# Kernel tuning notes

Hardware: AMD Instinct MI355X
Metric: run time of the kernel (lower is better)

The kernel has to match this reference:

```python
import jax, jax.numpy as jnp
import numpy as np

C = 512
GROUPS = 32
EPS = 1e-6


def setup_inputs() -> dict:
    key = jax.random.key(0)
    ks = jax.random.split(key, 10)
    s = 0.02
    return {
        "x": jax.random.normal(ks[0], (2, C, 64, 64), dtype=jnp.float32),
        "gn_scale": jnp.ones((C,), jnp.float32),
        "gn_bias": jnp.zeros((C,), jnp.float32),
        "wq": jax.random.normal(ks[1], (C, C), jnp.float32) * s,
        "bq": jnp.zeros((C,), jnp.float32),
        "wk": jax.random.normal(ks[2], (C, C), jnp.float32) * s,
        "bk": jnp.zeros((C,), jnp.float32),
        "wv": jax.random.normal(ks[3], (C, C), jnp.float32) * s,
        "bv": jnp.zeros((C,), jnp.float32),
        "wo": jax.random.normal(ks[4], (C, C), jnp.float32) * s,
        "bo": jnp.zeros((C,), jnp.float32),
    }


def group_norm(x, scale, bias):
    # x: [b, c, h, w]; 32 groups over channel dim
    b, c, h, w = x.shape
    xg = x.reshape(b, GROUPS, c // GROUPS, h, w)
    mean = jnp.mean(xg, axis=(2, 3, 4), keepdims=True)
    var = jnp.var(xg, axis=(2, 3, 4), keepdims=True)
    xg = (xg - mean) * jax.lax.rsqrt(var + EPS)
    x = xg.reshape(b, c, h, w)
    return x * scale[None, :, None, None] + bias[None, :, None, None]


def reference(x, gn_scale, gn_bias, wq, bq, wk, bk, wv, bv, wo, bo):
    b, c, h, w = x.shape
    n = h * w
    hn = group_norm(x, gn_scale, gn_bias).reshape(b, c, n)  # [b,c,n]
    # 1x1 conv == channel matmul: out[b,o,n] = W[o,i] @ h[b,i,n] + bias
    q = jnp.einsum('oi,bin->bon', wq, hn) + bq[None, :, None]
    k = jnp.einsum('oi,bin->bon', wk, hn) + bk[None, :, None]
    v = jnp.einsum('oi,bin->bon', wv, hn) + bv[None, :, None]
    # weight[b, i, j] = q_i . k_j, softmax over j
    scale = int(c) ** (-0.5)
    weight = jnp.einsum('bci,bcj->bij', q, k) * scale  # [b,n,n]
    weight = jax.nn.softmax(weight, axis=2)
    # h[b,c,i] = sum_j v[b,c,j] * weight[b,i,j]
    out = jnp.einsum('bcj,bij->bci', v, weight)
    out = jnp.einsum('oi,bin->bon', wo, out) + bo[None, :, None]
    return out.reshape(b, c, h, w) + x
```

## Files before the change

kernel.cpp:

```cpp
#include <hip/hip_runtime.h>
#include <hip/hip_bf16.h>


typedef __attribute__((ext_vector_type(8))) short short8_t;
typedef __attribute__((ext_vector_type(4))) short short4_t;
typedef __attribute__((ext_vector_type(4))) float f32x4;

__device__ __forceinline__ void gload16(const void* g, void* l) {
  __builtin_amdgcn_global_load_lds(
      (const __attribute__((address_space(1))) void*)g,
      (__attribute__((address_space(3))) void*)l, 16, 0, 0);
}

__device__ __forceinline__ short f2bf_bits(float f) {
  __hip_bfloat16 h = __float2bfloat16(f);
  return *reinterpret_cast<short*>(&h);
}
__device__ __forceinline__ float bfbits2f(short s) {
  union { unsigned int u; float f; } c;
  c.u = ((unsigned int)(unsigned short)s) << 16;
  return c.f;
}

__global__ __launch_bounds__(512)
void s_gemm8(const __hip_bfloat16* __restrict__ qk,
             __hip_bfloat16* __restrict__ P, float* __restrict__ part2,
             float c)
{
  const long long QKz = 4096LL * 1024;
  const long long SS  = 4096LL * 4096;

  const int b = blockIdx.x;
  const int bz = b >> 8;
  const int r = b & 255, xcd = r & 7, sl = r >> 3;
  const int bm = (xcd >> 1) * 4 + (sl & 3);
  const int bn = (xcd & 1) * 8 + (sl >> 2);

  const __hip_bfloat16* Aq = qk + (size_t)bz * QKz;
  const __hip_bfloat16* Bk = Aq + 512;

  const int tid = threadIdx.x;
  const int wid = tid >> 6, l = tid & 63;
  const int wrM = wid >> 2, wcN = wid & 3;
  const int lhi = l >> 4, llo = l & 15;

  __shared__ char sm[2 * 65536];

  f32x4 acc[2][2][4][2] = {};
  short8_t af[4][2], bf[2][2];

  const int rIn = l >> 3;
  const int colSw = 8 * ((l & 7) ^ (rIn & 7));
  const __hip_bfloat16* gA = Aq + (size_t)(bm * 256 + rIn) * 1024 + colSw;
  const __hip_bfloat16* gB = Bk + (size_t)(bn * 256 + rIn) * 1024 + colSw;

  auto STG = [&](int mat, int half, int t) {
    const __hip_bfloat16* src = mat ? gB : gA;
    char* dst = sm + (t & 1) * 65536 + mat * 32768;
    const int rb = half * 128 + wid * 16;
    gload16(src + (size_t)rb * 1024 + t * 64, dst + rb * 128);
    gload16(src + (size_t)(rb + 8) * 1024 + t * 64, dst + (rb + 8) * 128);
  };

#define PHASE(MH, NH, LA, LB, VM, ...) do {                                   \
    const char* bbA = sm + bsel * 65536;                                      \
    const char* bbB = bbA + 32768;                                            \
    if (LA) {                                                                 \
      _Pragma("unroll") for (int m = 0; m < 4; ++m) {                         \
        const int rowA = (MH) * 128 + wrM * 64 + m * 16 + llo;                \
        _Pragma("unroll") for (int kk = 0; kk < 2; ++kk)                      \
          af[m][kk] = *(const short8_t*)(bbA + rowA * 128 +                   \
                        (((kk * 4 + lhi) ^ (rowA & 7)) * 16));                \
      }                                                                       \
    }                                                                         \
    if (LB) {                                                                 \
      _Pragma("unroll") for (int n = 0; n < 2; ++n) {                         \
        const int rowB = (NH) * 128 + wcN * 32 + n * 16 + llo;                \
        _Pragma("unroll") for (int kk = 0; kk < 2; ++kk)                      \
          bf[n][kk] = *(const short8_t*)(bbB + rowB * 128 +                   \
                        (((kk * 4 + lhi) ^ (rowB & 7)) * 16));                \
      }                                                                       \
    }                                                                         \
    __VA_ARGS__;                                                              \
    __builtin_amdgcn_s_barrier();                                             \
    __builtin_amdgcn_s_setprio(1);                                            \
    _Pragma("unroll") for (int kk = 0; kk < 2; ++kk)                          \
      _Pragma("unroll") for (int m = 0; m < 4; ++m)                           \
        _Pragma("unroll") for (int n = 0; n < 2; ++n)                         \
          acc[MH][NH][m][n] = __builtin_amdgcn_mfma_f32_16x16x32_bf16(        \
              af[m][kk], bf[n][kk], acc[MH][NH][m][n], 0, 0, 0);              \
    __builtin_amdgcn_s_setprio(0);                                            \
    if ((VM) == 1) asm volatile("s_waitcnt vmcnt(4)" ::: "memory");           \
    if ((VM) == 2) asm volatile("s_waitcnt vmcnt(0)" ::: "memory");           \
    __builtin_amdgcn_s_barrier();                                             \
  } while (0)

  STG(0, 0, 0); STG(1, 0, 0); STG(0, 1, 0); STG(1, 1, 0);
  STG(0, 0, 1); STG(1, 0, 1); STG(0, 1, 1); STG(1, 1, 1);
  asm volatile("s_waitcnt vmcnt(0)" ::: "memory");
  __builtin_amdgcn_s_barrier();

  for (int t = 0; t < 8; ++t) {
    const int bsel = t & 1;
    const int stB = (t >= 1 && t < 7);
    const int stA = (t < 6);
    const int vm = (t < 6) ? 1 : (t == 6) ? 2 : 0;
    PHASE(0, 0, 1, 1, 0, if (stB) { STG(1, 0, t + 1); STG(1, 1, t + 1); });
    PHASE(0, 1, 0, 1, 0, if (stA) STG(0, 0, t + 2););
    PHASE(1, 1, 1, 0, 0, );
    PHASE(1, 0, 0, 1, vm, if (stA) STG(0, 1, t + 2););
  }
#undef PHASE

  __hip_bfloat16* Pb = P + (size_t)bz * SS;
  float rp[2][4][4];
#pragma unroll
  for (int Mh = 0; Mh < 2; ++Mh)
#pragma unroll
    for (int m = 0; m < 4; ++m)
#pragma unroll
      for (int rr = 0; rr < 4; ++rr) {
        const int grow = bm * 256 + Mh * 128 + wrM * 64 + m * 16 + lhi * 4 + rr;
        float s = 0.f;
#pragma unroll
        for (int Nh = 0; Nh < 2; ++Nh)
#pragma unroll
          for (int n = 0; n < 2; ++n) {
            const int gcol = bn * 256 + Nh * 128 + wcN * 32 + n * 16 + llo;
            const float v = exp2f(acc[Mh][Nh][m][n][rr] * c);
            Pb[(size_t)grow * 4096 + gcol] = __float2bfloat16(v);
            s += v;
          }
        rp[Mh][m][rr] = s;
      }
#pragma unroll
  for (int Mh = 0; Mh < 2; ++Mh)
#pragma unroll
    for (int m = 0; m < 4; ++m)
#pragma unroll
      for (int rr = 0; rr < 4; ++rr) {
        float s = rp[Mh][m][rr];
        s += __shfl_xor(s, 1); s += __shfl_xor(s, 2);
        s += __shfl_xor(s, 4); s += __shfl_xor(s, 8);
        rp[Mh][m][rr] = s;
      }
  __syncthreads();
  float* rsl = (float*)sm;
  if (llo == 0) {
#pragma unroll
    for (int Mh = 0; Mh < 2; ++Mh)
#pragma unroll
      for (int m = 0; m < 4; ++m)
#pragma unroll
        for (int rr = 0; rr < 4; ++rr) {
          const int rl = Mh * 128 + wrM * 64 + m * 16 + lhi * 4 + rr;
          rsl[rl * 4 + wcN] = rp[Mh][m][rr];
        }
  }
  __syncthreads();
  if (tid < 256) {
    const float s = rsl[tid * 4] + rsl[tid * 4 + 1] + rsl[tid * 4 + 2] + rsl[tid * 4 + 3];
    part2[((size_t)bz * 16 + bn) * 4096 + bm * 256 + tid] = s;
  }
}

__global__ __launch_bounds__(256)
void rs_final(const float* __restrict__ part2, float* __restrict__ rs)
{
  const int i = blockIdx.x * 256 + threadIdx.x;
  const int z = i >> 12, row = i & 4095;
  float s = 0.f;
#pragma unroll
  for (int bn = 0; bn < 16; ++bn)
    s += part2[((size_t)z * 16 + bn) * 4096 + row];
  rs[(size_t)z * 4096 + row] = 1.f / s;
}

template<int OUTF, int BIASMODE, int RESID, int PIPE, int MF, int NORM>
__device__ __forceinline__ void gemm_body(
    const __hip_bfloat16* __restrict__ A,
    const __hip_bfloat16* __restrict__ B,
    void* __restrict__ Cv,
    const float* __restrict__ bias,
    const float* __restrict__ resid,
    const float* __restrict__ rn,
    float scale, int K, int lda, int ldb, int ldc,
    long long strC, long long strR,
    int bm, int bn, int z, char* sm)
{
  constexpr int BUFSZ = MF * 4096 + 16384;
  const int tid = threadIdx.x;
  const int w = tid >> 6, l = tid & 63;
  const int wr = w >> 1, wc = w & 1;
  const int lhi = l >> 4, llo = l & 15;
  const int m0 = bm * (MF * 32), n0 = bn * 128;

  f32x4 acc[MF][4] = {};

  const int rowInCh = l >> 3;
  const int colOff = 8 * ((l & 7) ^ (rowInCh & 7));

  const __hip_bfloat16* gAr[MF];
  const __hip_bfloat16* gBr[4];
#pragma unroll
  for (int j = 0; j < MF; ++j)
    gAr[j] = A + (size_t)(m0 + w * (8 * MF) + j * 8 + rowInCh) * lda + colOff;
#pragma unroll
  for (int r = 0; r < 4; ++r)
    gBr[r] = B + (size_t)(n0 + w * 32 + r * 8 + rowInCh) * ldb + colOff;

  auto stage = [&](int kt, int buf) {
    char* sA = sm + buf * BUFSZ;
    char* sB = sA + MF * 4096;
    const int ko = kt * 64;
#pragma unroll
    for (int j = 0; j < MF; ++j)
      gload16(gAr[j] + ko, sA + (w * MF + j) * 1024);
#pragma unroll
    for (int r = 0; r < 4; ++r)
      gload16(gBr[r] + ko, sB + (w * 4 + r) * 1024);
  };

  auto compute = [&](int buf) {
    char* sA = sm + buf * BUFSZ;
    char* sB = sA + MF * 4096;
#pragma unroll
    for (int kk = 0; kk < 2; ++kk) {
      short8_t af[MF], bfv[4];
#pragma unroll
      for (int m = 0; m < MF; ++m) {
        const int row = wr * (16 * MF) + m * 16 + llo;
        const int inner = ((kk * 4 + lhi) ^ (row & 7)) * 16;
        af[m] = *(const short8_t*)(sA + row * 128 + inner);
      }
#pragma unroll
      for (int n = 0; n < 4; ++n) {
        const int row = wc * 64 + n * 16 + llo;
        const int inner = ((kk * 4 + lhi) ^ (row & 7)) * 16;
        bfv[n] = *(const short8_t*)(sB + row * 128 + inner);
      }
#pragma unroll
      for (int m = 0; m < MF; ++m)
#pragma unroll
        for (int n = 0; n < 4; ++n)
          acc[m][n] = __builtin_amdgcn_mfma_f32_16x16x32_bf16(af[m], bfv[n], acc[m][n], 0, 0, 0);
    }
  };

  const int nkt = K >> 6;
  if (PIPE) {
    stage(0, 0);
    __syncthreads();
    int cur = 0;
    for (int kt = 0; kt < nkt; ++kt) {
      if (kt + 1 < nkt) stage(kt + 1, cur ^ 1);
      compute(cur);
      __syncthreads();
      cur ^= 1;
    }
  } else {
    for (int kt = 0; kt < nkt; ++kt) {
      __syncthreads();
      stage(kt, 0);
      __syncthreads();
      compute(0);
    }
  }

#pragma unroll
  for (int m = 0; m < MF; ++m) {
#pragma unroll
    for (int r = 0; r < 4; ++r) {
      const int grow = m0 + wr * (16 * MF) + m * 16 + lhi * 4 + r;
#pragma unroll
      for (int n = 0; n < 4; ++n) {
        const int gcol = n0 + wc * 64 + n * 16 + llo;
        float v = acc[m][n][r] * scale;
        if (NORM == 1) v *= rn[(size_t)z * 4096 + gcol];
        if (BIASMODE == 1) v += bias[grow];
        if (BIASMODE == 2) v += bias[gcol];
        const size_t idx = (size_t)z * strC + (size_t)grow * ldc + gcol;
        if (RESID) v += resid[(size_t)z * strR + (size_t)grow * ldc + gcol];
        if (OUTF == 0) ((__hip_bfloat16*)Cv)[idx] = __float2bfloat16(v);
        else           ((float*)Cv)[idx] = v;
      }
    }
  }
}

template<int OUTF, int BIASMODE, int RESID, int PIPE, int SWZ, int MF, int NORM>
__global__ __launch_bounds__(256, 2)
void gemm_nt(const __hip_bfloat16* __restrict__ A,
             const __hip_bfloat16* __restrict__ B,
             void* __restrict__ Cv,
             const float* __restrict__ bias,
             const float* __restrict__ resid,
             const float* __restrict__ rn,
             float scale, int M, int N, int K,
             int lda, int ldb, int ldc,
             long long strA, long long strB, long long strC, long long strR)
{
  int bm, bn, bz;
  if (SWZ == 0) {
    bm = blockIdx.x; bn = blockIdx.y; bz = blockIdx.z;
  } else if (SWZ == 2) {
    const int b = blockIdx.x;
    bz = b >> 10;
    const int b2 = b & 1023;
    const int xcd = b2 & 7, s = b2 >> 3;
    bm = (xcd >> 1) * 8 + (s & 7);
    bn = (xcd & 1) * 16 + (s >> 3);
  } else {
    const int b = blockIdx.x;
    const int xcd = b & 7, slot = b >> 3;
    bm = slot & 7;
    const int panel = xcd * 8 + (slot >> 3);
    bn = panel & 31; bz = panel >> 5;
  }
  __shared__ char sm[(PIPE ? 2 : 1) * (MF * 4096 + 16384)];
  gemm_body<OUTF, BIASMODE, RESID, PIPE, MF, NORM>(
      A + (size_t)bz * strA, B + (size_t)bz * strB, Cv, bias, resid, rn,
      scale, K, lda, ldb, ldc, strC, strR, bm, bn, bz, sm);
}

__global__ __launch_bounds__(256, 2)
void qkvo(const __hip_bfloat16* __restrict__ ht,
          const __hip_bfloat16* __restrict__ wqk,
          const __hip_bfloat16* __restrict__ wvo,
          __hip_bfloat16* __restrict__ qk,
          __hip_bfloat16* __restrict__ vo,
          const float* __restrict__ bqk)
{
  const long long HT  = 4096LL * 512;
  const long long QKz = 4096LL * 1024;
  const long long VOz = 512LL * 4096;
  __shared__ char sm[65536];
  const int b = blockIdx.x;
  if (b < 512) {
    const int bm = b & 31, bn = (b >> 5) & 7, bz = b >> 8;
    gemm_body<0, 2, 0, 1, 4, 0>(
        ht + (size_t)bz * HT, wqk, qk, bqk, nullptr, nullptr,
        1.f, 512, 512, 512, 1024, QKz, 0, bm, bn, bz, sm);
  } else {
    const int b2 = b - 512;
    const int xcd = b2 & 7, slot = b2 >> 3;
    const int bm = slot & 7;
    const int panel = xcd * 8 + (slot >> 3);
    const int bn = panel & 31, bz = panel >> 5;
    gemm_body<0, 0, 0, 1, 2, 0>(
        wvo, ht + (size_t)bz * HT, vo, nullptr, nullptr, nullptr,
        1.f, 512, 512, 512, 4096, VOz, 0, bm, bn, bz, sm);
  }
}

__global__ __launch_bounds__(256)
void prep_all(const float* __restrict__ wq, const float* __restrict__ wk,
              const float* __restrict__ wo, const float* __restrict__ wv,
              const float* __restrict__ bv, const float* __restrict__ bo,
              const float* __restrict__ bq, const float* __restrict__ bk,
              const float* __restrict__ x,
              __hip_bfloat16* __restrict__ wbf, __hip_bfloat16* __restrict__ wvT,
              float* __restrict__ bvo, float* __restrict__ bqk,
              float* __restrict__ part)
{
  const int b = blockIdx.x, tid = threadIdx.x;
  if (b < 768) {
    const int j = b >> 8;
    const float* src = (j == 0) ? wq : (j == 1) ? wk : wo;
    const int i = (b & 255) * 256 + tid;
    float4 v = reinterpret_cast<const float4*>(src)[i];
    short4_t o;
    o[0] = f2bf_bits(v.x); o[1] = f2bf_bits(v.y);
    o[2] = f2bf_bits(v.z); o[3] = f2bf_bits(v.w);
    *reinterpret_cast<short4_t*>((short*)wbf + (size_t)j * 262144 + (size_t)i * 4) = o;
  } else if (b < 832) {
    __shared__ float tile[64][65];
    const int b2 = b - 768, ct = b2 >> 3, it = b2 & 7;
    const int lane = tid & 63, rr = tid >> 6;
#pragma unroll
    for (int p = 0; p < 16; ++p) {
      const int cl = p * 4 + rr;
      tile[cl][lane] = wv[(size_t)(ct * 64 + cl) * 512 + it * 64 + lane];
    }
    __syncthreads();
#pragma unroll
    for (int p = 0; p < 16; ++p) {
      const int il = p * 4 + rr;
      wvT[(size_t)(it * 64 + il) * 512 + ct * 64 + lane] = __float2bfloat16(tile[lane][il]);
    }
  } else if (b < 834) {
    const int o = (b - 832) * 256 + tid;
    const float4* row = reinterpret_cast<const float4*>(wo + (size_t)o * 512);
    const float4* b4 = reinterpret_cast<const float4*>(bv);
    float s = 0.f;
#pragma unroll 8
    for (int i = 0; i < 128; ++i) {
      float4 a = row[i], bb = b4[i];
      s += a.x * bb.x + a.y * bb.y + a.z * bb.z + a.w * bb.w;
    }
    bvo[o] = s + bo[o];
    bqk[o] = bq[o];
    bqk[512 + o] = bk[o];
  } else {
    const int b3 = b - 834;
    const int g = b3 & 31, sl = (b3 >> 5) & 15, z = b3 >> 9;
    const float* xf = x + (size_t)z * 512 * 4096 + (size_t)g * 16 * 4096 + (size_t)sl * 4096;
    const float4* px = reinterpret_cast<const float4*>(xf);
    float s = 0.f, q = 0.f;
#pragma unroll
    for (int i = 0; i < 4; ++i) {
      float4 v = px[tid + i * 256];
      s += v.x + v.y + v.z + v.w;
      q += v.x * v.x + v.y * v.y + v.z * v.z + v.w * v.w;
    }
#pragma unroll
    for (int o = 32; o; o >>= 1) { s += __shfl_xor(s, o); q += __shfl_xor(q, o); }
    __shared__ float rs[4], rq[4];
    if ((tid & 63) == 0) { rs[tid >> 6] = s; rq[tid >> 6] = q; }
    __syncthreads();
    if (tid == 0) {
      s = rs[0] + rs[1] + rs[2] + rs[3];
      q = rq[0] + rq[1] + rq[2] + rq[3];
      part[(((size_t)z * 32 + g) * 16 + sl) * 2 + 0] = s;
      part[(((size_t)z * 32 + g) * 16 + sl) * 2 + 1] = q;
    }
  }
}

__global__ __launch_bounds__(256)
void gn_apply_t(const float* __restrict__ x, const float* __restrict__ part,
                const float* __restrict__ gns, const float* __restrict__ gnb,
                __hip_bfloat16* __restrict__ ht)
{
  const int st = blockIdx.x, ct = blockIdx.y, z = blockIdx.z;
  const int tid = threadIdx.x;
  __shared__ float tile[64][65];
  __shared__ float smean[4], srstd[4];
  if (tid < 4) {
    const int g = ct * 4 + tid;
    float s = 0.f, q = 0.f;
#pragma unroll
    for (int slc = 0; slc < 16; ++slc) {
      s += part[(((size_t)z * 32 + g) * 16 + slc) * 2 + 0];
      q += part[(((size_t)z * 32 + g) * 16 + slc) * 2 + 1];
    }
    const float mean = s * (1.0f / 65536.0f);
    const float var = q * (1.0f / 65536.0f) - mean * mean;
    smean[tid] = mean;
    srstd[tid] = rsqrtf(var + 1e-6f);
  }
  __syncthreads();
  const float* xb = x + (size_t)z * 512 * 4096;
  const int lane64 = tid & 63, rr = tid >> 6;
#pragma unroll
  for (int pp = 0; pp < 16; ++pp) {
    const int cl = pp * 4 + rr;
    const int c = ct * 64 + cl;
    const float val = xb[(size_t)c * 4096 + st * 64 + lane64];
    tile[cl][lane64] = (val - smean[cl >> 4]) * srstd[cl >> 4] * gns[c] + gnb[c];
  }
  __syncthreads();
  __hip_bfloat16* hb = ht + (size_t)z * 4096 * 512;
#pragma unroll
  for (int pp = 0; pp < 16; ++pp) {
    const int sl = pp * 4 + rr;
    const int s = st * 64 + sl;
    hb[(size_t)s * 512 + ct * 64 + lane64] = __float2bfloat16(tile[lane64][sl]);
  }
}

__global__ __launch_bounds__(256)
void softmax_rows(__hip_bfloat16* __restrict__ S, long long strZ)
{
  const int row = blockIdx.x, z = blockIdx.y;
  __hip_bfloat16* p = S + (size_t)z * strZ + (size_t)row * 4096;
  const int tid = threadIdx.x;
  short8_t a = *(const short8_t*)(p + tid * 16);
  short8_t b = *(const short8_t*)(p + tid * 16 + 8);
  float v[16];
#pragma unroll
  for (int i = 0; i < 8; ++i) { v[i] = bfbits2f(a[i]); v[8 + i] = bfbits2f(b[i]); }
  float m = v[0];
#pragma unroll
  for (int i = 1; i < 16; ++i) m = fmaxf(m, v[i]);
#pragma unroll
  for (int o = 32; o; o >>= 1) m = fmaxf(m, __shfl_xor(m, o));
  __shared__ float red[8];
  if ((tid & 63) == 0) red[tid >> 6] = m;
  __syncthreads();
  m = fmaxf(fmaxf(red[0], red[1]), fmaxf(red[2], red[3]));
  float s = 0.f;
#pragma unroll
  for (int i = 0; i < 16; ++i) { v[i] = exp2f((v[i] - m) * 1.44269504f); s += v[i]; }
#pragma unroll
  for (int o = 32; o; o >>= 1) s += __shfl_xor(s, o);
  __syncthreads();
  if ((tid & 63) == 0) red[4 + (tid >> 6)] = s;
  __syncthreads();
  s = red[4] + red[5] + red[6] + red[7];
  const float inv = 1.f / s;
#pragma unroll
  for (int i = 0; i < 8; ++i) { a[i] = f2bf_bits(v[i] * inv); b[i] = f2bf_bits(v[8 + i] * inv); }
  *(short8_t*)(p + tid * 16) = a;
  *(short8_t*)(p + tid * 16 + 8) = b;
}

extern "C" void kernel_launch(void* const* d_in, const int* in_sizes, int n_in,
                              void* d_out, int out_size, void* d_ws, size_t ws_size,
                              hipStream_t stream)
{
  const float* x   = (const float*)d_in[0];
  const float* gns = (const float*)d_in[1];
  const float* gnb = (const float*)d_in[2];
  const float* wq  = (const float*)d_in[3];
  const float* bq  = (const float*)d_in[4];
  const float* wk  = (const float*)d_in[5];
  const float* bk  = (const float*)d_in[6];
  const float* wv  = (const float*)d_in[7];
  const float* bv  = (const float*)d_in[8];
  const float* wo  = (const float*)d_in[9];
  const float* bo  = (const float*)d_in[10];
  float* out = (float*)d_out;

  const int WB = 512 * 512;
  const long long HT  = 4096LL * 512;
  const long long QKz = 4096LL * 1024;
  const long long VOz = 512LL * 4096;
  const long long SS  = 4096LL * 4096;
  const long long CHW = 512LL * 4096;

  char* base = (char*)d_ws;
  size_t off = 0;
  auto alloc = [&](size_t b) { void* r = base + off; off = (off + b + 255) & ~(size_t)255; return r; };

  __hip_bfloat16* wbf = (__hip_bfloat16*)alloc((size_t)5 * WB * 2);
  float* bqk   = (float*)alloc(1024 * 4);
  float* bvo   = (float*)alloc(512 * 4);
  float* part  = (float*)alloc(2 * 32 * 16 * 2 * 4);
  float* rsum  = (float*)alloc(2 * 4096 * 4);
  float* part2 = (float*)alloc((size_t)2 * 16 * 4096 * 4);
  const size_t fixed = off;

  const size_t qkB = (size_t)2 * QKz * 2;
  const size_t voB = (size_t)2 * VOz * 2;
  const size_t sB2 = (size_t)2 * SS * 2;
  const size_t sB1 = (size_t)SS * 2;
  const int MODE = (ws_size >= fixed + qkB + voB + sB2) ? 2 : 1;

  __hip_bfloat16* qk   = (__hip_bfloat16*)alloc(qkB);
  __hip_bfloat16* vo   = (__hip_bfloat16*)alloc(voB);
  const size_t sbufB = (MODE == 2) ? sB2 : sB1;
  __hip_bfloat16* sbuf = (__hip_bfloat16*)alloc(sbufB);
  __hip_bfloat16* ht = (__hip_bfloat16*)((char*)sbuf + sbufB - (size_t)2 * HT * 2);

  __hip_bfloat16* wqk = wbf;
  __hip_bfloat16* woB = wbf + 2 * WB;
  __hip_bfloat16* wvT = wbf + 3 * WB;
  __hip_bfloat16* wvo = wbf + 4 * WB;

  const float SC = 0.04419417382415922f;
  const float CEXP = SC * 1.4426950408889634f;

  prep_all<<<1858, 256, 0, stream>>>(wq, wk, wo, wv, bv, bo, bq, bk, x,
                                     wbf, wvT, bvo, bqk, part);

  gemm_nt<0, 0, 0, 1, 0, 4, 0><<<dim3(4, 4, 1), 256, 0, stream>>>(
      woB, wvT, wvo, nullptr, nullptr, nullptr, 1.f, 512, 512, 512,
      512, 512, 512, 0, 0, 0, 0);

  gn_apply_t<<<dim3(64, 8, 2), 256, 0, stream>>>(x, part, gns, gnb, ht);

  if (MODE == 2) {
    qkvo<<<1024, 256, 0, stream>>>(ht, wqk, wvo, qk, vo, bqk);
    s_gemm8<<<512, 512, 0, stream>>>(qk, sbuf, part2, CEXP);
    rs_final<<<32, 256, 0, stream>>>(part2, rsum);
    gemm_nt<1, 1, 1, 1, 3, 2, 1><<<dim3(512, 1, 1), 256, 0, stream>>>(
        vo, sbuf, out, bvo, x, rsum, 1.f, 512, 4096, 4096,
        4096, 4096, 4096, VOz, SS, CHW, CHW);
  } else {
    gemm_nt<0, 2, 0, 1, 0, 4, 0><<<dim3(32, 8, 2), 256, 0, stream>>>(
        ht, wqk, qk, bqk, nullptr, nullptr, 1.f, 4096, 1024, 512,
        512, 512, 1024, HT, 0, QKz, 0);
    gemm_nt<0, 0, 0, 1, 3, 2, 0><<<dim3(512, 1, 1), 256, 0, stream>>>(
        wvo, ht, vo, nullptr, nullptr, nullptr, 1.f, 512, 4096, 512,
        512, 512, 4096, 0, HT, VOz, 0);
    for (int z = 0; z < 2; ++z) {
      gemm_nt<0, 0, 0, 0, 0, 4, 0><<<dim3(32, 32, 1), 256, 0, stream>>>(
          qk + (size_t)z * QKz, qk + (size_t)z * QKz + 512, sbuf, nullptr, nullptr,
          nullptr, SC, 4096, 4096, 512, 1024, 1024, 4096, 0, 0, 0, 0);
      softmax_rows<<<dim3(4096, 1), 256, 0, stream>>>(sbuf, 0);
      gemm_nt<1, 1, 1, 1, 0, 2, 0><<<dim3(8, 32, 1), 256, 0, stream>>>(
          vo + (size_t)z * VOz, sbuf, out + (size_t)z * CHW, bvo, x + (size_t)z * CHW,
          nullptr, 1.f, 512, 4096, 4096, 4096, 4096, 4096, 0, 0, 0, 0);
    }
  }
}
```

Measured before the change: 145.6 us.

## Switch attention QK, P and PV paths to FP8 e4m3 MFMA

Q/K and V·O projections now emit FP8 e4m3 bytes, the score GEMM uses fp8 MFMA with half the K-steps, and the exponentiated probabilities are stored as FP8. A new dedicated pv_fp8 kernel multiplies FP8 V by FP8 P and applies the normalisation, bias and residual. This halves memory traffic for the large 4096x4096 P matrix and uses the higher-throughput FP8 MFMA path. In exchange it costs precision, which could exceed tolerance, and uses a software float-to-e4m3 conversion on every store.

```diff
diff --git a/kernel.cpp b/kernel.cpp
--- a/kernel.cpp
+++ b/kernel.cpp
@@ -22,10 +22,33 @@
   return c.f;
 }
 
+__device__ __forceinline__ unsigned char f2e4m3(float f) {
+  union { float f; unsigned int u; } a; a.f = f;
+  const unsigned char s = (a.u >> 24) & 0x80;
+  a.u &= 0x7FFFFFFFu;
+  if (a.f >= 448.f) return s | 0x7E;
+  if (a.f < 0.0009765625f) return s;
+  const int exp = (int)(a.u >> 23) - 127;
+  if (exp >= -6) {
+    unsigned int keep = (a.u >> 20) & 7;
+    const unsigned int rest = a.u & 0xFFFFF;
+    int e = exp;
+    keep += (rest > 0x80000u) || (rest == 0x80000u && (keep & 1));
+    if (keep == 8) { keep = 0; ++e; }
+    unsigned int enc = ((unsigned int)(e + 7) << 3) | keep;
+    if (enc >= 0x7F) enc = 0x7E;
+    return s | (unsigned char)enc;
+  }
+  const float scaled = a.f * 512.f;
+  int q = (int)(scaled + 0.5f);
+  if (q >= 8) return s | 0x08;
+  return s | (unsigned char)q;
+}
+
 __global__ __launch_bounds__(512)
-void s_gemm8(const __hip_bfloat16* __restrict__ qk,
-             __hip_bfloat16* __restrict__ P, float* __restrict__ part2,
-             float c)
+void s_gemm8f(const unsigned char* __restrict__ qk,
+              unsigned char* __restrict__ P, float* __restrict__ part2,
+              float c)
 {
   const long long QKz = 4096LL * 1024;
   const long long SS  = 4096LL * 4096;
@@ -36,8 +59,8 @@
   const int bm = (xcd >> 1) * 4 + (sl & 3);
   const int bn = (xcd & 1) * 8 + (sl >> 2);
 
-  const __hip_bfloat16* Aq = qk + (size_t)bz * QKz;
-  const __hip_bfloat16* Bk = Aq + 512;
+  const unsigned char* Aq = qk + (size_t)bz * QKz;
+  const unsigned char* Bk = Aq + 512;
 
   const int tid = threadIdx.x;
   const int wid = tid >> 6, l = tid & 63;
@@ -47,19 +70,19 @@
   __shared__ char sm[2 * 65536];
 
   f32x4 acc[2][2][4][2] = {};
-  short8_t af[4][2], bf[2][2];
+  long long af[4][4], bf[2][4];
 
   const int rIn = l >> 3;
-  const int colSw = 8 * ((l & 7) ^ (rIn & 7));
-  const __hip_bfloat16* gA = Aq + (size_t)(bm * 256 + rIn) * 1024 + colSw;
-  const __hip_bfloat16* gB = Bk + (size_t)(bn * 256 + rIn) * 1024 + colSw;
+  const int colSw = 16 * ((l & 7) ^ (rIn & 7));
+  const unsigned char* gA = Aq + (size_t)(bm * 256 + rIn) * 1024 + colSw;
+  const unsigned char* gB = Bk + (size_t)(bn * 256 + rIn) * 1024 + colSw;
 
   auto STG = [&](int mat, int half, int t) {
-    const __hip_bfloat16* src = mat ? gB : gA;
+    const unsigned char* src = mat ? gB : gA;
     char* dst = sm + (t & 1) * 65536 + mat * 32768;
     const int rb = half * 128 + wid * 16;
-    gload16(src + (size_t)rb * 1024 + t * 64, dst + rb * 128);
-    gload16(src + (size_t)(rb + 8) * 1024 + t * 64, dst + (rb + 8) * 128);
+    gload16(src + (size_t)rb * 1024 + t * 128, dst + rb * 128);
+    gload16(src + (size_t)(rb + 8) * 1024 + t * 128, dst + (rb + 8) * 128);
   };
 
 #define PHASE(MH, NH, LA, LB, VM, ...) do {                                   \
@@ -68,26 +91,26 @@
     if (LA) {                                                                 \
       _Pragma("unroll") for (int m = 0; m < 4; ++m) {                         \
         const int rowA = (MH) * 128 + wrM * 64 + m * 16 + llo;                \
-        _Pragma("unroll") for (int kk = 0; kk < 2; ++kk)                      \
-          af[m][kk] = *(const short8_t*)(bbA + rowA * 128 +                   \
-                        (((kk * 4 + lhi) ^ (rowA & 7)) * 16));                \
+        _Pragma("unroll") for (int kk = 0; kk < 4; ++kk)                      \
+          af[m][kk] = *(const long long*)(bbA + rowA * 128 +                  \
+              (((kk * 2 + (lhi >> 1)) ^ (rowA & 7)) * 16) + (lhi & 1) * 8);   \
       }                                                                       \
     }                                                                         \
     if (LB) {                                                                 \
       _Pragma("unroll") for (int n = 0; n < 2; ++n) {                         \
         const int rowB = (NH) * 128 + wcN * 32 + n * 16 + llo;                \
-        _Pragma("unroll") for (int kk = 0; kk < 2; ++kk)                      \
-          bf[n][kk] = *(const short8_t*)(bbB + rowB * 128 +                   \
-                        (((kk * 4 + lhi) ^ (rowB & 7)) * 16));                \
+        _Pragma("unroll") for (int kk = 0; kk < 4; ++kk)                      \
+          bf[n][kk] = *(const long long*)(bbB + rowB * 128 +                  \
+              (((kk * 2 + (lhi >> 1)) ^ (rowB & 7)) * 16) + (lhi & 1) * 8);   \
       }                                                                       \
     }                                                                         \
     __VA_ARGS__;                                                              \
     __builtin_amdgcn_s_barrier();                                             \
     __builtin_amdgcn_s_setprio(1);                                            \
-    _Pragma("unroll") for (int kk = 0; kk < 2; ++kk)                          \
+    _Pragma("unroll") for (int kk = 0; kk < 4; ++kk)                          \
       _Pragma("unroll") for (int m = 0; m < 4; ++m)                           \
         _Pragma("unroll") for (int n = 0; n < 2; ++n)                         \
-          acc[MH][NH][m][n] = __builtin_amdgcn_mfma_f32_16x16x32_bf16(        \
+          acc[MH][NH][m][n] = __builtin_amdgcn_mfma_f32_16x16x32_fp8_fp8(     \
               af[m][kk], bf[n][kk], acc[MH][NH][m][n], 0, 0, 0);              \
     __builtin_amdgcn_s_setprio(0);                                            \
     if ((VM) == 1) asm volatile("s_waitcnt vmcnt(4)" ::: "memory");           \
@@ -100,11 +123,11 @@
   asm volatile("s_waitcnt vmcnt(0)" ::: "memory");
   __builtin_amdgcn_s_barrier();
 
-  for (int t = 0; t < 8; ++t) {
+  for (int t = 0; t < 4; ++t) {
     const int bsel = t & 1;
-    const int stB = (t >= 1 && t < 7);
-    const int stA = (t < 6);
-    const int vm = (t < 6) ? 1 : (t == 6) ? 2 : 0;
+    const int stB = (t >= 1 && t < 3);
+    const int stA = (t < 2);
+    const int vm = (t < 2) ? 1 : (t == 2) ? 2 : 0;
     PHASE(0, 0, 1, 1, 0, if (stB) { STG(1, 0, t + 1); STG(1, 1, t + 1); });
     PHASE(0, 1, 0, 1, 0, if (stA) STG(0, 0, t + 2););
     PHASE(1, 1, 1, 0, 0, );
@@ -112,7 +135,7 @@
   }
 #undef PHASE
 
-  __hip_bfloat16* Pb = P + (size_t)bz * SS;
+  unsigned char* Pb = P + (size_t)bz * SS;
   float rp[2][4][4];
 #pragma unroll
   for (int Mh = 0; Mh < 2; ++Mh)
@@ -128,7 +151,7 @@
           for (int n = 0; n < 2; ++n) {
             const int gcol = bn * 256 + Nh * 128 + wcN * 32 + n * 16 + llo;
             const float v = exp2f(acc[Mh][Nh][m][n][rr] * c);
-            Pb[(size_t)grow * 4096 + gcol] = __float2bfloat16(v);
+            Pb[(size_t)grow * 4096 + gcol] = f2e4m3(v);
             s += v;
           }
         rp[Mh][m][rr] = s;
@@ -174,6 +197,116 @@
   for (int bn = 0; bn < 16; ++bn)
     s += part2[((size_t)z * 16 + bn) * 4096 + row];
   rs[(size_t)z * 4096 + row] = 1.f / s;
+}
+
+__global__ __launch_bounds__(256, 2)
+void pv_fp8(const unsigned char* __restrict__ VOp,
+            const unsigned char* __restrict__ P,
+            float* __restrict__ out,
+            const float* __restrict__ bvo,
+            const float* __restrict__ x,
+            const float* __restrict__ rsum)
+{
+  const long long VOz = 512LL * 4096;
+  const long long SS  = 4096LL * 4096;
+  const long long CHW = 512LL * 4096;
+
+  const int b = blockIdx.x;
+  const int xcd = b & 7, slot = b >> 3;
+  const int bm = slot & 7;
+  const int panel = xcd * 8 + (slot >> 3);
+  const int bn = panel & 31, bz = panel >> 5;
+
+  const unsigned char* A = VOp + (size_t)bz * VOz;
+  const unsigned char* B = P + (size_t)bz * SS;
+
+  const int tid = threadIdx.x;
+  const int w = tid >> 6, l = tid & 63;
+  const int wr = w >> 1, wc = w & 1;
+  const int lhi = l >> 4, llo = l & 15;
+  const int m0 = bm * 64, n0 = bn * 128;
+
+  constexpr int BUFSZ = 8192 + 16384;
+  __shared__ char sm[2 * BUFSZ];
+
+  f32x4 acc[2][4] = {};
+
+  const int rIn = l >> 3;
+  const int colSw = 16 * ((l & 7) ^ (rIn & 7));
+
+  const unsigned char* gAr[2];
+  const unsigned char* gBr[4];
+#pragma unroll
+  for (int j = 0; j < 2; ++j)
+    gAr[j] = A + (size_t)(m0 + w * 16 + j * 8 + rIn) * 4096 + colSw;
+#pragma unroll
+  for (int r = 0; r < 4; ++r)
+    gBr[r] = B + (size_t)(n0 + w * 32 + r * 8 + rIn) * 4096 + colSw;
+
+  auto stage = [&](int kt, int buf) {
+    char* sA = sm + buf * BUFSZ;
+    char* sB = sA + 8192;
+    const int ko = kt * 128;
+#pragma unroll
+    for (int j = 0; j < 2; ++j)
+      gload16(gAr[j] + ko, sA + (w * 2 + j) * 1024);
+#pragma unroll
+    for (int r = 0; r < 4; ++r)
+      gload16(gBr[r] + ko, sB + (w * 4 + r) * 1024);
+  };
+
+  auto compute = [&](int buf) {
+    char* sA = sm + buf * BUFSZ;
+    char* sB = sA + 8192;
+#pragma unroll
+    for (int kk = 0; kk < 4; ++kk) {
+      long long afv[2], bfv[4];
+#pragma unroll
+      for (int m = 0; m < 2; ++m) {
+        const int row = wr * 32 + m * 16 + llo;
+        afv[m] = *(const long long*)(sA + row * 128 +
+            (((kk * 2 + (lhi >> 1)) ^ (row & 7)) * 16) + (lhi & 1) * 8);
+      }
+#pragma unroll
+      for (int n = 0; n < 4; ++n) {
+        const int row = wc * 64 + n * 16 + llo;
+        bfv[n] = *(const long long*)(sB + row * 128 +
+            (((kk * 2 + (lhi >> 1)) ^ (row & 7)) * 16) + (lhi & 1) * 8);
+      }
+#pragma unroll
+      for (int m = 0; m < 2; ++m)
+#pragma unroll
+        for (int n = 0; n < 4; ++n)
+          acc[m][n] = __builtin_amdgcn_mfma_f32_16x16x32_fp8_fp8(
+              afv[m], bfv[n], acc[m][n], 0, 0, 0);
+    }
+  };
+
+  const int nkt = 32;
+  stage(0, 0);
+  __syncthreads();
+  int cur = 0;
+  for (int kt = 0; kt < nkt; ++kt) {
+    if (kt + 1 < nkt) stage(kt + 1, cur ^ 1);
+    compute(cur);
+    __syncthreads();
+    cur ^= 1;
+  }
+
+#pragma unroll
+  for (int m = 0; m < 2; ++m) {
+#pragma unroll
+    for (int r = 0; r < 4; ++r) {
+      const int grow = m0 + wr * 32 + m * 16 + lhi * 4 + r;
+#pragma unroll
+      for (int n = 0; n < 4; ++n) {
+        const int gcol = n0 + wc * 64 + n * 16 + llo;
+        float v = acc[m][n][r] * rsum[(size_t)bz * 4096 + gcol] + bvo[grow];
+        v += x[(size_t)bz * CHW + (size_t)grow * 4096 + gcol];
+        out[(size_t)bz * CHW + (size_t)grow * 4096 + gcol] = v;
+      }
+    }
+  }
 }
 
 template<int OUTF, int BIASMODE, int RESID, int PIPE, int MF, int NORM>
@@ -281,8 +414,9 @@
         if (BIASMODE == 2) v += bias[gcol];
         const size_t idx = (size_t)z * strC + (size_t)grow * ldc + gcol;
         if (RESID) v += resid[(size_t)z * strR + (size_t)grow * ldc + gcol];
-        if (OUTF == 0) ((__hip_bfloat16*)Cv)[idx] = __float2bfloat16(v);
-        else           ((float*)Cv)[idx] = v;
+        if (OUTF == 0)      ((__hip_bfloat16*)Cv)[idx] = __float2bfloat16(v);
+        else if (OUTF == 1) ((float*)Cv)[idx] = v;
+        else                ((unsigned char*)Cv)[idx] = f2e4m3(v);
       }
     }
   }
@@ -303,13 +437,6 @@
   int bm, bn, bz;
   if (SWZ == 0) {
     bm = blockIdx.x; bn = blockIdx.y; bz = blockIdx.z;
-  } else if (SWZ == 2) {
-    const int b = blockIdx.x;
-    bz = b >> 10;
-    const int b2 = b & 1023;
-    const int xcd = b2 & 7, s = b2 >> 3;
-    bm = (xcd >> 1) * 8 + (s & 7);
-    bn = (xcd & 1) * 16 + (s >> 3);
   } else {
     const int b = blockIdx.x;
     const int xcd = b & 7, slot = b >> 3;
@@ -327,8 +454,8 @@
 void qkvo(const __hip_bfloat16* __restrict__ ht,
           const __hip_bfloat16* __restrict__ wqk,
           const __hip_bfloat16* __restrict__ wvo,
-          __hip_bfloat16* __restrict__ qk,
-          __hip_bfloat16* __restrict__ vo,
+          unsigned char* __restrict__ qk8,
+          unsigned char* __restrict__ vo8,
           const float* __restrict__ bqk)
 {
   const long long HT  = 4096LL * 512;
@@ -338,8 +465,8 @@
   const int b = blockIdx.x;
   if (b < 512) {
     const int bm = b & 31, bn = (b >> 5) & 7, bz = b >> 8;
-    gemm_body<0, 2, 0, 1, 4, 0>(
-        ht + (size_t)bz * HT, wqk, qk, bqk, nullptr, nullptr,
+    gemm_body<2, 2, 0, 1, 4, 0>(
+        ht + (size_t)bz * HT, wqk, qk8, bqk, nullptr, nullptr,
         1.f, 512, 512, 512, 1024, QKz, 0, bm, bn, bz, sm);
   } else {
     const int b2 = b - 512;
@@ -347,8 +474,8 @@
     const int bm = slot & 7;
     const int panel = xcd * 8 + (slot >> 3);
     const int bn = panel & 31, bz = panel >> 5;
-    gemm_body<0, 0, 0, 1, 2, 0>(
-        wvo, ht + (size_t)bz * HT, vo, nullptr, nullptr, nullptr,
+    gemm_body<2, 0, 0, 1, 2, 0>(
+        wvo, ht + (size_t)bz * HT, vo8, nullptr, nullptr, nullptr,
         1.f, 512, 512, 512, 4096, VOz, 0, bm, bn, bz, sm);
   }
 }
@@ -541,17 +668,8 @@
   float* part2 = (float*)alloc((size_t)2 * 16 * 4096 * 4);
   const size_t fixed = off;
 
-  const size_t qkB = (size_t)2 * QKz * 2;
-  const size_t voB = (size_t)2 * VOz * 2;
-  const size_t sB2 = (size_t)2 * SS * 2;
-  const size_t sB1 = (size_t)SS * 2;
-  const int MODE = (ws_size >= fixed + qkB + voB + sB2) ? 2 : 1;
-
-  __hip_bfloat16* qk   = (__hip_bfloat16*)alloc(qkB);
-  __hip_bfloat16* vo   = (__hip_bfloat16*)alloc(voB);
-  const size_t sbufB = (MODE == 2) ? sB2 : sB1;
-  __hip_bfloat16* sbuf = (__hip_bfloat16*)alloc(sbufB);
-  __hip_bfloat16* ht = (__hip_bfloat16*)((char*)sbuf + sbufB - (size_t)2 * HT * 2);
+  const int MODE = (ws_size >= fixed + (size_t)2 * QKz + (size_t)2 * VOz +
+                    (size_t)2 * SS + (size_t)4 * HT) ? 2 : 1;
 
   __hip_bfloat16* wqk = wbf;
   __hip_bfloat16* woB = wbf + 2 * WB;
@@ -568,16 +686,24 @@
       woB, wvT, wvo, nullptr, nullptr, nullptr, 1.f, 512, 512, 512,
       512, 512, 512, 0, 0, 0, 0);
 
-  gn_apply_t<<<dim3(64, 8, 2), 256, 0, stream>>>(x, part, gns, gnb, ht);
-
   if (MODE == 2) {
-    qkvo<<<1024, 256, 0, stream>>>(ht, wqk, wvo, qk, vo, bqk);
-    s_gemm8<<<512, 512, 0, stream>>>(qk, sbuf, part2, CEXP);
+    unsigned char* qk8  = (unsigned char*)alloc((size_t)2 * QKz);
+    unsigned char* vo8  = (unsigned char*)alloc((size_t)2 * VOz);
+    unsigned char* p8   = (unsigned char*)alloc((size_t)2 * SS);
+    __hip_bfloat16* ht = (__hip_bfloat16*)(p8 + (size_t)2 * SS - (size_t)4 * HT);
+
+    gn_apply_t<<<dim3(64, 8, 2), 256, 0, stream>>>(x, part, gns, gnb, ht);
+    qkvo<<<1024, 256, 0, stream>>>(ht, wqk, wvo, qk8, vo8, bqk);
+    s_gemm8f<<<512, 512, 0, stream>>>(qk8, p8, part2, CEXP);
     rs_final<<<32, 256, 0, stream>>>(part2, rsum);
-    gemm_nt<1, 1, 1, 1, 3, 2, 1><<<dim3(512, 1, 1), 256, 0, stream>>>(
-        vo, sbuf, out, bvo, x, rsum, 1.f, 512, 4096, 4096,
-        4096, 4096, 4096, VOz, SS, CHW, CHW);
+    pv_fp8<<<512, 256, 0, stream>>>(vo8, p8, out, bvo, x, rsum);
   } else {
+    __hip_bfloat16* qk   = (__hip_bfloat16*)alloc((size_t)2 * QKz * 2);
+    __hip_bfloat16* vo   = (__hip_bfloat16*)alloc((size_t)2 * VOz * 2);
+    __hip_bfloat16* sbuf = (__hip_bfloat16*)alloc((size_t)SS * 2);
+    __hip_bfloat16* ht   = (__hip_bfloat16*)((char*)sbuf + (size_t)SS * 2 - (size_t)4 * HT);
+
+    gn_apply_t<<<dim3(64, 8, 2), 256, 0, stream>>>(x, part, gns, gnb, ht);
     gemm_nt<0, 2, 0, 1, 0, 4, 0><<<dim3(32, 8, 2), 256, 0, stream>>>(
         ht, wqk, qk, bqk, nullptr, nullptr, 1.f, 4096, 1024, 512,
         512, 512, 1024, HT, 0, QKz, 0);
```

Result: slower. 185.1 us (+27.1%).
